# Kernel tuning notes

Hardware: AMD Instinct MI355X
Metric: run time of the kernel (lower is better)

Reference implementation:

```python
import jax, jax.numpy as jnp
import numpy as np

N, H, W = 8, 64, 64
CIN = 512    # latent_size_prev == conv_insize
COUT = 512   # latent_size == conv_outsize
Z = 512      # latent vector dim


def setup_inputs() -> dict:
    key = jax.random.key(0)
    ks = jax.random.split(key, 6)
    data = jax.random.normal(ks[0], (N, H, W, CIN), dtype=jnp.float32)
    latent = jax.random.normal(ks[1], (N, Z), dtype=jnp.float32)
    dense_w = jax.random.normal(ks[2], (Z, CIN), dtype=jnp.float32)
    dense_b = jnp.ones((CIN,), dtype=jnp.float32)  # ones_initializer per StyleBlock2
    conv_w = jax.random.normal(ks[3], (3, 3, CIN, COUT), dtype=jnp.float32)
    bias = jnp.zeros((1, 1, 1, COUT), dtype=jnp.float32)
    noise_coef = jnp.zeros((1, 1, 1, COUT), dtype=jnp.float32)
    noise = jax.random.normal(ks[4], (N, H, W, COUT), dtype=jnp.float32)
    return {"data": data, "latent": latent, "dense_w": dense_w, "dense_b": dense_b,
            "conv_w": conv_w, "bias": bias, "noise_coef": noise_coef, "noise": noise}


def reference(data, latent, dense_w, dense_b, conv_w, bias, noise_coef, noise):
    # ScaledDense: style vector s = latent @ (W * sqrt(2/Z)) + b
    dense_coef = jnp.sqrt(2.0 / Z).astype(data.dtype)
    s = latent @ (dense_w * dense_coef) + dense_b           # [N, CIN]

    # modulate input by style
    x = data * s[:, None, None, :]                          # [N,H,W,CIN]

    conv_coef = jnp.sqrt(2.0 / (CIN * 9)).astype(data.dtype)
    w = conv_w * conv_coef                                  # [3,3,CIN,COUT]
    y = jax.lax.conv_general_dilated(
        x, w, window_strides=(1, 1), padding='SAME',
        dimension_numbers=('NHWC', 'HWIO', 'NHWC'))         # [N,H,W,COUT]

    # demodulation: sum_{k,k,cin} (w * s)^2 == (s^2) @ sum_{k,k} w^2
    w2 = jnp.sum(w * w, axis=(0, 1))                        # [CIN, COUT]
    d = jax.lax.rsqrt((s * s) @ w2 + 1e-8)                  # [N, COUT]
    y = y * d[:, None, None, :]

    y = y + bias + noise * noise_coef
    return jnp.where(y >= 0, y, 0.2 * y)  # leaky relu, alpha=0.2
```

## Files before the change

kernel.cpp:

```cpp
#include <hip/hip_runtime.h>
#include <stdint.h>

typedef unsigned short ushort_t;
typedef unsigned int uint_t;
typedef __bf16 bf16x8 __attribute__((ext_vector_type(8)));
typedef float f32x4 __attribute__((ext_vector_type(4)));

#define C2F 0.02083333333333333f

__device__ __forceinline__ float bf2f(unsigned short u) {
  union { unsigned int i; float f; } v; v.i = ((unsigned int)u) << 16; return v.f;
}
__device__ __forceinline__ unsigned short f2bf(float f) {
  union { float f; unsigned int i; } v; v.f = f;
  unsigned int r = v.i + 0x7FFFu + ((v.i >> 16) & 1u);
  return (unsigned short)(r >> 16);
}
__device__ __forceinline__ bool bf_mode(const void* dense_b) {
  return *(const uint_t*)dense_b == 0x3F803F80u;
}
__device__ __forceinline__ void async16(const void* g, void* l) {
  __builtin_amdgcn_global_load_lds(
      (const __attribute__((address_space(1))) unsigned int*)g,
      (__attribute__((address_space(3))) unsigned int*)l, 16, 0, 0);
}

__global__ void k_style_p(const void* __restrict__ latent, const void* __restrict__ dw,
                          const void* __restrict__ db, float* __restrict__ sp) {
  const bool bf = bf_mode(db);
  int c = blockIdx.x * 256 + threadIdx.x;
  int n = blockIdx.y, zc = blockIdx.z;
  int z0 = zc * 64;
  float acc = 0.f;
  if (bf) {
    const ushort_t* L = (const ushort_t*)latent;
    const ushort_t* W = (const ushort_t*)dw;
    for (int z = z0; z < z0 + 64; ++z) acc += bf2f(L[n * 512 + z]) * bf2f(W[z * 512 + c]);
  } else {
    const float* L = (const float*)latent;
    const float* W = (const float*)dw;
    for (int z = z0; z < z0 + 64; ++z) acc += L[n * 512 + z] * W[z * 512 + c];
  }
  sp[(zc * 8 + n) * 512 + c] = acc;
}

__global__ void k_style_f(const float* __restrict__ sp, const void* __restrict__ db,
                          float* __restrict__ s) {
  const bool bf = bf_mode(db);
  int c = blockIdx.x * 256 + threadIdx.x;
  int n = blockIdx.y;
  float acc = 0.f;
#pragma unroll
  for (int zc = 0; zc < 8; ++zc) acc += sp[(zc * 8 + n) * 512 + c];
  float bv = bf ? bf2f(((const ushort_t*)db)[c]) : ((const float*)db)[c];
  s[n * 512 + c] = acc * 0.0625f + bv;
}

__global__ void k_w2(const void* __restrict__ cw, const void* __restrict__ db,
                     float* __restrict__ w2) {
  const bool bf = bf_mode(db);
  int i = blockIdx.x * blockDim.x + threadIdx.x;
  float a = 0.f;
  if (bf) {
    const ushort_t* W = (const ushort_t*)cw;
    for (int t = 0; t < 9; ++t) { float v = bf2f(W[t * 262144 + i]); a += v * v; }
  } else {
    const float* W = (const float*)cw;
    for (int t = 0; t < 9; ++t) { float v = W[t * 262144 + i]; a += v * v; }
  }
  w2[i] = a;
}

__global__ void k_demod_p(const float* __restrict__ s, const float* __restrict__ w2,
                          float* __restrict__ qp) {
  int c = blockIdx.x * 256 + threadIdx.x;
  int n = blockIdx.y, kc = blockIdx.z;
  int k0 = kc * 64;
  float q = 0.f;
  for (int k = k0; k < k0 + 64; ++k) {
    float sv = s[n * 512 + k];
    q += sv * sv * w2[k * 512 + c];
  }
  qp[(kc * 8 + n) * 512 + c] = q;
}

__global__ void k_demod_f(const float* __restrict__ qp, float* __restrict__ dfac) {
  int c = blockIdx.x * 256 + threadIdx.x;
  int n = blockIdx.y;
  float q = 0.f;
#pragma unroll
  for (int kc = 0; kc < 8; ++kc) q += qp[(kc * 8 + n) * 512 + c];
  dfac[n * 512 + c] = C2F * rsqrtf(C2F * C2F * q + 1e-8f);
}

__global__ void k_wt(const void* __restrict__ cw, const void* __restrict__ db,
                     ushort_t* __restrict__ wT) {
  __shared__ ushort_t tile[64][66];
  const bool bf = bf_mode(db);
  int tap = blockIdx.z;
  int ci0 = blockIdx.y * 64, co0 = blockIdx.x * 64;
  int col = threadIdx.x & 63, r0 = threadIdx.x >> 6;
  if (bf) {
    const ushort_t* src = (const ushort_t*)cw + tap * 262144;
    for (int r = r0; r < 64; r += 4) tile[r][col] = src[(ci0 + r) * 512 + co0 + col];
  } else {
    const float* src = (const float*)cw + tap * 262144;
    for (int r = r0; r < 64; r += 4) tile[r][col] = f2bf(src[(ci0 + r) * 512 + co0 + col]);
  }
  __syncthreads();
  ushort_t* dst = wT + tap * 262144;
  for (int r = r0; r < 64; r += 4)
    dst[(co0 + r) * 512 + ci0 + col] = tile[col][r];
}

__global__ void k_xpad(const void* __restrict__ data, const void* __restrict__ db,
                       const float* __restrict__ s, ushort_t* __restrict__ xpad) {
  const bool bf = bf_mode(db);
  int idx = blockIdx.x * blockDim.x + threadIdx.x;
  int cpair = idx & 255;
  int p = idx >> 8;
  int wp = p % 66; int q = p / 66; int hp = q % 66; int n = q / 66;
  uint_t outv = 0u;
  if ((unsigned)(hp - 1) < 64u && (unsigned)(wp - 1) < 64u) {
    int c = cpair * 2;
    int src = ((n * 64 + (hp - 1)) * 64 + (wp - 1)) * 512 + c;
    float s0 = s[n * 512 + c], s1 = s[n * 512 + c + 1];
    float x0, x1;
    if (bf) {
      uint_t dp = *(const uint_t*)((const ushort_t*)data + src);
      x0 = bf2f((unsigned short)(dp & 0xFFFFu)) * s0;
      x1 = bf2f((unsigned short)(dp >> 16)) * s1;
    } else {
      const float* df = (const float*)data;
      x0 = df[src] * s0;
      x1 = df[src + 1] * s1;
    }
    outv = (uint_t)f2bf(x0) | ((uint_t)f2bf(x1) << 16);
  }
  *(uint_t*)(xpad + idx * 2) = outv;
}

template <bool BF>
__device__ __forceinline__ void do_epilogue(
    const f32x4 (&acc)[4][4], const float* __restrict__ dfac,
    const void* __restrict__ bias, const void* __restrict__ ncoef,
    const void* __restrict__ noise, void* __restrict__ out,
    int n_img, int posBase, int coutBase, int lane, int wm, int wn) {
  const int rowq = (lane >> 4) * 4;
#pragma unroll
  for (int j = 0; j < 4; ++j) {
    const int cout = coutBase + wn + j * 16 + (lane & 15);
    const float dv = dfac[n_img * 512 + cout];
    const float bv = BF ? bf2f(((const ushort_t*)bias)[cout]) : ((const float*)bias)[cout];
    const float nc = BF ? bf2f(((const ushort_t*)ncoef)[cout]) : ((const float*)ncoef)[cout];
#pragma unroll
    for (int i = 0; i < 4; ++i) {
      const int m = wm + i * 16 + rowq;
#pragma unroll
      for (int r = 0; r < 4; ++r) {
        const size_t o = (size_t)(posBase + m + r) * 512 + cout;
        const float nv = BF ? bf2f(((const ushort_t*)noise)[o]) : ((const float*)noise)[o];
        float y = acc[i][j][r] * dv + bv + nv * nc;
        y = (y >= 0.f) ? y : 0.2f * y;
        if (BF) ((ushort_t*)out)[o] = f2bf(y);
        else    ((float*)out)[o] = y;
      }
    }
  }
}

__global__ __launch_bounds__(256, 2) void k_conv(
    const ushort_t* __restrict__ xpad, const ushort_t* __restrict__ wT,
    const float* __restrict__ dfac, const void* __restrict__ bias,
    const void* __restrict__ ncoef, const void* __restrict__ noise,
    const void* __restrict__ db, void* __restrict__ out) {
  __shared__ ushort_t Asm[128 * 32];
  __shared__ ushort_t Bsm[128 * 32];

  const int t = threadIdx.x;
  const int bid = blockIdx.x;
  const int xcd = bid & 7;
  const int slot = bid >> 3;
  const int coutBase = (slot & 3) * 128;
  const int posBase = ((slot >> 2) + 32 * xcd) * 128;
  const int n_img = posBase >> 12;

  const int prow = t >> 2;
  const int kch = (t & 3) * 8;
  const int pos0 = posBase + prow;
  const int pos1 = pos0 + 64;
  const int h0 = (pos0 >> 6) & 63, w0c = pos0 & 63;
  const int h1 = (pos1 >> 6) & 63, w1c = pos1 & 63;
  const ushort_t* gA0 = xpad + ((n_img * 66 + h0) * 66 + w0c) * 512 + kch;
  const ushort_t* gA1 = xpad + ((n_img * 66 + h1) * 66 + w1c) * 512 + kch;
  const ushort_t* gB0 = wT + (coutBase + prow) * 512 + kch;
  const ushort_t* gB1 = gB0 + 64 * 512;
  ushort_t* lA0 = Asm + t * 8;
  ushort_t* lA1 = lA0 + 64 * 32;
  ushort_t* lB0 = Bsm + t * 8;
  ushort_t* lB1 = lB0 + 64 * 32;

  const int lane = t & 63;
  const int wm = ((t >> 7) & 1) * 64;
  const int wn = ((t >> 6) & 1) * 64;
  const int mrow = lane & 15;
  const int kreg = (lane >> 4) * 8;

  f32x4 acc[4][4] = {};

  for (int tap = 0; tap < 9; ++tap) {
    const int kh = tap / 3, kw = tap - kh * 3;
    const ushort_t* pA0 = gA0 + (kh * 66 + kw) * 512;
    const ushort_t* pA1 = gA1 + (kh * 66 + kw) * 512;
    const ushort_t* pB0 = gB0 + tap * 262144;
    const ushort_t* pB1 = gB1 + tap * 262144;
    for (int k0 = 0; k0 < 512; k0 += 32) {
      async16(pA0 + k0, lA0);
      async16(pA1 + k0, lA1);
      async16(pB0 + k0, lB0);
      async16(pB1 + k0, lB1);
      asm volatile("s_waitcnt vmcnt(0)" ::: "memory");
      __syncthreads();
      bf16x8 av[4], bv[4];
#pragma unroll
      for (int i = 0; i < 4; ++i)
        av[i] = *(const bf16x8*)(Asm + (wm + i * 16 + mrow) * 32 + kreg);
#pragma unroll
      for (int j = 0; j < 4; ++j)
        bv[j] = *(const bf16x8*)(Bsm + (wn + j * 16 + mrow) * 32 + kreg);
#pragma unroll
      for (int i = 0; i < 4; ++i)
#pragma unroll
        for (int j = 0; j < 4; ++j)
          acc[i][j] = __builtin_amdgcn_mfma_f32_16x16x32_bf16(av[i], bv[j], acc[i][j], 0, 0, 0);
      __syncthreads();
    }
  }

  if (bf_mode(db))
    do_epilogue<true>(acc, dfac, bias, ncoef, noise, out, n_img, posBase, coutBase, lane, wm, wn);
  else
    do_epilogue<false>(acc, dfac, bias, ncoef, noise, out, n_img, posBase, coutBase, lane, wm, wn);
}

extern "C" void kernel_launch(void* const* d_in, const int* in_sizes, int n_in,
                              void* d_out, int out_size, void* d_ws, size_t ws_size,
                              hipStream_t stream) {
  (void)in_sizes; (void)n_in; (void)out_size; (void)ws_size;
  const void* data    = d_in[0];
  const void* latent  = d_in[1];
  const void* dense_w = d_in[2];
  const void* dense_b = d_in[3];
  const void* conv_w  = d_in[4];
  const void* bias    = d_in[5];
  const void* ncoef   = d_in[6];
  const void* noise   = d_in[7];

  float* s    = (float*)d_ws;
  float* dfac = s + 4096;
  float* w2   = dfac + 4096;
  float* sp   = w2 + 262144;
  float* qp   = sp + 32768;
  ushort_t* wT   = (ushort_t*)(qp + 32768);
  ushort_t* xpad = wT + 2359296;

  k_style_p<<<dim3(2, 8, 8), 256, 0, stream>>>(latent, dense_w, dense_b, sp);
  k_style_f<<<dim3(2, 8), 256, 0, stream>>>(sp, dense_b, s);
  k_w2<<<1024, 256, 0, stream>>>(conv_w, dense_b, w2);
  k_wt<<<dim3(8, 8, 9), 256, 0, stream>>>(conv_w, dense_b, wT);
  k_demod_p<<<dim3(2, 8, 8), 256, 0, stream>>>(s, w2, qp);
  k_demod_f<<<dim3(2, 8), 256, 0, stream>>>(qp, dfac);
  k_xpad<<<34848, 256, 0, stream>>>(data, dense_b, s, xpad);
  k_conv<<<1024, 256, 0, stream>>>(xpad, wT, dfac, bias, ncoef, noise, dense_b, d_out);
}
```

Baseline: 437.1 us.

## Rewrite implicit-GEMM conv with 256x256 tiles, double-buffered swizzled LDS pipeline

The conv kernel moves from 128x128 tiles with a single-buffered 32-wide K loop to 256x256 tiles across 8 waves. It uses K-steps of 64, double-buffered XOR-swizzled LDS (128KB dynamic), and interleaves async global-to-LDS staging with MFMA phases using partial vmcnt waits and setprio. The padded-input prep kernel is also vectorized to 8 channels per thread. The aim is to hide load latency, cut barrier stalls and raise data reuse. In exchange it uses much more LDS and registers, and launches only 256 blocks.

```diff
diff --git a/kernel.cpp b/kernel.cpp
--- a/kernel.cpp
+++ b/kernel.cpp
@@ -116,51 +116,63 @@
 __global__ void k_xpad(const void* __restrict__ data, const void* __restrict__ db,
                        const float* __restrict__ s, ushort_t* __restrict__ xpad) {
   const bool bf = bf_mode(db);
-  int idx = blockIdx.x * blockDim.x + threadIdx.x;
-  int cpair = idx & 255;
-  int p = idx >> 8;
+  int idx = blockIdx.x * 256 + threadIdx.x;
+  int c = (idx & 63) * 8;
+  int p = idx >> 6;
   int wp = p % 66; int q = p / 66; int hp = q % 66; int n = q / 66;
-  uint_t outv = 0u;
+  uint_t ov[4] = {0u, 0u, 0u, 0u};
   if ((unsigned)(hp - 1) < 64u && (unsigned)(wp - 1) < 64u) {
-    int c = cpair * 2;
-    int src = ((n * 64 + (hp - 1)) * 64 + (wp - 1)) * 512 + c;
-    float s0 = s[n * 512 + c], s1 = s[n * 512 + c + 1];
-    float x0, x1;
+    const float4 s0 = *(const float4*)(s + n * 512 + c);
+    const float4 s1 = *(const float4*)(s + n * 512 + c + 4);
+    size_t src = (size_t)((n * 64 + (hp - 1)) * 64 + (wp - 1)) * 512 + c;
+    float x[8];
     if (bf) {
-      uint_t dp = *(const uint_t*)((const ushort_t*)data + src);
-      x0 = bf2f((unsigned short)(dp & 0xFFFFu)) * s0;
-      x1 = bf2f((unsigned short)(dp >> 16)) * s1;
+      uint4 dv = *(const uint4*)((const ushort_t*)data + src);
+      x[0] = bf2f((unsigned short)(dv.x & 0xFFFFu)); x[1] = bf2f((unsigned short)(dv.x >> 16));
+      x[2] = bf2f((unsigned short)(dv.y & 0xFFFFu)); x[3] = bf2f((unsigned short)(dv.y >> 16));
+      x[4] = bf2f((unsigned short)(dv.z & 0xFFFFu)); x[5] = bf2f((unsigned short)(dv.z >> 16));
+      x[6] = bf2f((unsigned short)(dv.w & 0xFFFFu)); x[7] = bf2f((unsigned short)(dv.w >> 16));
     } else {
-      const float* df = (const float*)data;
-      x0 = df[src] * s0;
-      x1 = df[src + 1] * s1;
+      const float* df = (const float*)data + src;
+      float4 a = *(const float4*)df; float4 b = *(const float4*)(df + 4);
+      x[0] = a.x; x[1] = a.y; x[2] = a.z; x[3] = a.w;
+      x[4] = b.x; x[5] = b.y; x[6] = b.z; x[7] = b.w;
     }
-    outv = (uint_t)f2bf(x0) | ((uint_t)f2bf(x1) << 16);
-  }
-  *(uint_t*)(xpad + idx * 2) = outv;
+    float sv[8] = {s0.x, s0.y, s0.z, s0.w, s1.x, s1.y, s1.z, s1.w};
+#pragma unroll
+    for (int j = 0; j < 4; ++j)
+      ov[j] = (uint_t)f2bf(x[j * 2] * sv[j * 2]) |
+              ((uint_t)f2bf(x[j * 2 + 1] * sv[j * 2 + 1]) << 16);
+  }
+  uint4 o; o.x = ov[0]; o.y = ov[1]; o.z = ov[2]; o.w = ov[3];
+  *(uint4*)(xpad + (size_t)p * 512 + c) = o;
 }
 
 template <bool BF>
-__device__ __forceinline__ void do_epilogue(
-    const f32x4 (&acc)[4][4], const float* __restrict__ dfac,
+__device__ __forceinline__ void epi(
+    const f32x4 (&acc)[2][4][2][2], const float* __restrict__ dfac,
     const void* __restrict__ bias, const void* __restrict__ ncoef,
     const void* __restrict__ noise, void* __restrict__ out,
-    int n_img, int posBase, int coutBase, int lane, int wm, int wn) {
-  const int rowq = (lane >> 4) * 4;
-#pragma unroll
-  for (int j = 0; j < 4; ++j) {
-    const int cout = coutBase + wn + j * 16 + (lane & 15);
+    int n_img, int posBase, int coutBase, int lane, int wr, int wc) {
+  const int rq = (lane >> 4) * 4;
+#pragma unroll
+  for (int nh = 0; nh < 2; ++nh)
+#pragma unroll
+  for (int fn = 0; fn < 2; ++fn) {
+    const int cout = coutBase + wc * 64 + nh * 32 + fn * 16 + (lane & 15);
     const float dv = dfac[n_img * 512 + cout];
     const float bv = BF ? bf2f(((const ushort_t*)bias)[cout]) : ((const float*)bias)[cout];
     const float nc = BF ? bf2f(((const ushort_t*)ncoef)[cout]) : ((const float*)ncoef)[cout];
 #pragma unroll
-    for (int i = 0; i < 4; ++i) {
-      const int m = wm + i * 16 + rowq;
+    for (int mh = 0; mh < 2; ++mh)
+#pragma unroll
+    for (int f = 0; f < 4; ++f) {
+      const int m = wr * 128 + mh * 64 + f * 16 + rq;
 #pragma unroll
       for (int r = 0; r < 4; ++r) {
         const size_t o = (size_t)(posBase + m + r) * 512 + cout;
         const float nv = BF ? bf2f(((const ushort_t*)noise)[o]) : ((const float*)noise)[o];
-        float y = acc[i][j][r] * dv + bv + nv * nc;
+        float y = acc[mh][f][nh][fn][r] * dv + bv + nv * nc;
         y = (y >= 0.f) ? y : 0.2f * y;
         if (BF) ((ushort_t*)out)[o] = f2bf(y);
         else    ((float*)out)[o] = y;
@@ -169,78 +181,120 @@
   }
 }
 
-__global__ __launch_bounds__(256, 2) void k_conv(
+__global__ __launch_bounds__(512, 2) void k_conv(
     const ushort_t* __restrict__ xpad, const ushort_t* __restrict__ wT,
     const float* __restrict__ dfac, const void* __restrict__ bias,
     const void* __restrict__ ncoef, const void* __restrict__ noise,
     const void* __restrict__ db, void* __restrict__ out) {
-  __shared__ ushort_t Asm[128 * 32];
-  __shared__ ushort_t Bsm[128 * 32];
+  extern __shared__ ushort_t lds[];
 
   const int t = threadIdx.x;
   const int bid = blockIdx.x;
-  const int xcd = bid & 7;
-  const int slot = bid >> 3;
-  const int coutBase = (slot & 3) * 128;
-  const int posBase = ((slot >> 2) + 32 * xcd) * 128;
+  const int coutBase = (bid & 1) * 256;
+  const int posBase = (bid >> 1) * 256;
   const int n_img = posBase >> 12;
-
-  const int prow = t >> 2;
-  const int kch = (t & 3) * 8;
-  const int pos0 = posBase + prow;
-  const int pos1 = pos0 + 64;
-  const int h0 = (pos0 >> 6) & 63, w0c = pos0 & 63;
-  const int h1 = (pos1 >> 6) & 63, w1c = pos1 & 63;
-  const ushort_t* gA0 = xpad + ((n_img * 66 + h0) * 66 + w0c) * 512 + kch;
-  const ushort_t* gA1 = xpad + ((n_img * 66 + h1) * 66 + w1c) * 512 + kch;
-  const ushort_t* gB0 = wT + (coutBase + prow) * 512 + kch;
-  const ushort_t* gB1 = gB0 + 64 * 512;
-  ushort_t* lA0 = Asm + t * 8;
-  ushort_t* lA1 = lA0 + 64 * 32;
-  ushort_t* lB0 = Bsm + t * 8;
-  ushort_t* lB1 = lB0 + 64 * 32;
-
-  const int lane = t & 63;
-  const int wm = ((t >> 7) & 1) * 64;
-  const int wn = ((t >> 6) & 1) * 64;
-  const int mrow = lane & 15;
-  const int kreg = (lane >> 4) * 8;
-
-  f32x4 acc[4][4] = {};
-
-  for (int tap = 0; tap < 9; ++tap) {
-    const int kh = tap / 3, kw = tap - kh * 3;
-    const ushort_t* pA0 = gA0 + (kh * 66 + kw) * 512;
-    const ushort_t* pA1 = gA1 + (kh * 66 + kw) * 512;
-    const ushort_t* pB0 = gB0 + tap * 262144;
-    const ushort_t* pB1 = gB1 + tap * 262144;
-    for (int k0 = 0; k0 < 512; k0 += 32) {
-      async16(pA0 + k0, lA0);
-      async16(pA1 + k0, lA1);
-      async16(pB0 + k0, lB0);
-      async16(pB1 + k0, lB1);
-      asm volatile("s_waitcnt vmcnt(0)" ::: "memory");
-      __syncthreads();
-      bf16x8 av[4], bv[4];
-#pragma unroll
-      for (int i = 0; i < 4; ++i)
-        av[i] = *(const bf16x8*)(Asm + (wm + i * 16 + mrow) * 32 + kreg);
-#pragma unroll
-      for (int j = 0; j < 4; ++j)
-        bv[j] = *(const bf16x8*)(Bsm + (wn + j * 16 + mrow) * 32 + kreg);
-#pragma unroll
-      for (int i = 0; i < 4; ++i)
-#pragma unroll
-        for (int j = 0; j < 4; ++j)
-          acc[i][j] = __builtin_amdgcn_mfma_f32_16x16x32_bf16(av[i], bv[j], acc[i][j], 0, 0, 0);
-      __syncthreads();
-    }
-  }
+  const int hh0 = (posBase >> 6) & 63;
+
+  const int rt = t >> 3;
+  const int c8 = ((t & 7) ^ (rt & 7)) * 8;
+  const ushort_t* aPtr = xpad + ((size_t)((n_img * 66 + hh0) * 66 + rt) * 512 + c8);
+  const int bRow = ((t >> 8) & 1) * 64 + ((t >> 3) & 31);
+  const ushort_t* bPtr = wT + ((size_t)(coutBase + bRow) * 512 + c8);
+  ushort_t* aLds = lds + t * 8;
+  ushort_t* bLds = lds + 32768 + t * 8;
+
+#define STG_A(slot, mh, kt) do { \
+    const int tap_ = (kt) >> 3, kh_ = tap_ / 3, kw_ = tap_ - kh_ * 3, k0_ = ((kt) & 7) << 6; \
+    async16(aPtr + ((((mh) + kh_) * 66 + kw_) * 512 + k0_), \
+            aLds + (slot) * 16384 + (mh) * 4096); \
+    async16(aPtr + ((((mh) + 2 + kh_) * 66 + kw_) * 512 + k0_), \
+            aLds + (slot) * 16384 + ((mh) + 2) * 4096); \
+  } while (0)
+#define STG_B(slot, nh, kt) do { \
+    const int tap_ = (kt) >> 3, k0_ = ((kt) & 7) << 6; \
+    async16(bPtr + (tap_ * 262144 + (nh) * 16384 + k0_), \
+            bLds + (slot) * 16384 + (nh) * 8192); \
+    async16(bPtr + (tap_ * 262144 + (nh) * 16384 + 65536 + k0_), \
+            bLds + (slot) * 16384 + (nh) * 8192 + 4096); \
+  } while (0)
+
+  STG_A(0, 0, 0); STG_B(0, 0, 0); STG_B(0, 1, 0); STG_A(0, 1, 0);
+  STG_A(1, 0, 1); STG_B(1, 0, 1); STG_B(1, 1, 1);
+
+  const int lane = t & 63, wid = t >> 6, wr = wid >> 2, wc = wid & 3;
+  const int g16 = (lane >> 4) * 16, lrow = lane & 15, xv = (lane & 7) << 4;
+  const char* LB = (const char*)lds;
+  const int sbA0 = (((wr * 128 + lrow) * 128) + g16) ^ xv;
+  const int sbA1 = (((wr * 128 + lrow) * 128) + 64 + g16) ^ xv;
+  const int sbB0 = ((65536 + (wc * 32 + lrow) * 128) + g16) ^ xv;
+  const int sbB1 = ((65536 + (wc * 32 + lrow) * 128) + 64 + g16) ^ xv;
+
+  bf16x8 rA[4][2], rB0[2][2], rB1[2][2];
+  f32x4 acc[2][4][2][2] = {};
+
+#define LDA(mh, sB) do { _Pragma("unroll") for (int f = 0; f < 4; ++f) { \
+    rA[f][0] = *(const bf16x8*)(LB + ((sB) + (mh) * 8192 + f * 2048 + sbA0)); \
+    rA[f][1] = *(const bf16x8*)(LB + ((sB) + (mh) * 8192 + f * 2048 + sbA1)); } } while (0)
+#define LDB(R, nh, sB) do { _Pragma("unroll") for (int fn = 0; fn < 2; ++fn) { \
+    R[fn][0] = *(const bf16x8*)(LB + ((sB) + (nh) * 16384 + fn * 2048 + sbB0)); \
+    R[fn][1] = *(const bf16x8*)(LB + ((sB) + (nh) * 16384 + fn * 2048 + sbB1)); } } while (0)
+#define MM(mh, nh, RB) do { __builtin_amdgcn_s_setprio(1); \
+    _Pragma("unroll") for (int f = 0; f < 4; ++f) \
+    _Pragma("unroll") for (int fn = 0; fn < 2; ++fn) \
+    _Pragma("unroll") for (int ks = 0; ks < 2; ++ks) \
+      acc[mh][f][nh][fn] = __builtin_amdgcn_mfma_f32_16x16x32_bf16( \
+          rA[f][ks], (RB)[fn][ks], acc[mh][f][nh][fn], 0, 0, 0); \
+    __builtin_amdgcn_s_setprio(0); } while (0)
+#define BAR()   asm volatile("s_barrier" ::: "memory")
+#define LGKM0() asm volatile("s_waitcnt lgkmcnt(0)" ::: "memory")
+#define WAITV6() asm volatile("s_waitcnt vmcnt(6)" ::: "memory")
+
+  WAITV6();
+  BAR();
+
+#pragma unroll 1
+  for (int it = 0; it < 36; ++it) {
+    const int kt0 = 2 * it;
+    const int ktA = kt0 + 1;
+    const int ktB = (kt0 + 2 <= 71) ? kt0 + 2 : 71;
+    const int ktC = (kt0 + 3 <= 71) ? kt0 + 3 : 71;
+    LDA(0, 0); LDB(rB0, 0, 0);
+    STG_A(1, 1, ktA);
+    BAR(); LGKM0(); MM(0, 0, rB0); BAR();
+    LDB(rB1, 1, 0);
+    STG_A(0, 0, ktB);
+    BAR(); LGKM0(); MM(0, 1, rB1); BAR();
+    LDA(1, 0);
+    STG_B(0, 0, ktB);
+    BAR(); LGKM0(); MM(1, 1, rB1); BAR();
+    STG_B(0, 1, ktB);
+    BAR(); MM(1, 0, rB0); WAITV6(); BAR();
+    LDA(0, 32768); LDB(rB0, 0, 32768);
+    STG_A(0, 1, ktB);
+    BAR(); LGKM0(); MM(0, 0, rB0); BAR();
+    LDB(rB1, 1, 32768);
+    STG_A(1, 0, ktC);
+    BAR(); LGKM0(); MM(0, 1, rB1); BAR();
+    LDA(1, 32768);
+    STG_B(1, 0, ktC);
+    BAR(); LGKM0(); MM(1, 1, rB1); BAR();
+    STG_B(1, 1, ktC);
+    BAR(); MM(1, 0, rB0); WAITV6(); BAR();
+  }
+  asm volatile("s_waitcnt vmcnt(0)" ::: "memory");
 
   if (bf_mode(db))
-    do_epilogue<true>(acc, dfac, bias, ncoef, noise, out, n_img, posBase, coutBase, lane, wm, wn);
+    epi<true>(acc, dfac, bias, ncoef, noise, out, n_img, posBase, coutBase, lane, wr, wc);
   else
-    do_epilogue<false>(acc, dfac, bias, ncoef, noise, out, n_img, posBase, coutBase, lane, wm, wn);
+    epi<false>(acc, dfac, bias, ncoef, noise, out, n_img, posBase, coutBase, lane, wr, wc);
+#undef STG_A
+#undef STG_B
+#undef LDA
+#undef LDB
+#undef MM
+#undef BAR
+#undef LGKM0
+#undef WAITV6
 }
 
 extern "C" void kernel_launch(void* const* d_in, const int* in_sizes, int n_in,
@@ -256,6 +310,13 @@
   const void* ncoef   = d_in[6];
   const void* noise   = d_in[7];
 
+  static int once = [] {
+    (void)hipFuncSetAttribute((const void*)k_conv,
+                              hipFuncAttributeMaxDynamicSharedMemorySize, 131072);
+    return 0;
+  }();
+  (void)once;
+
   float* s    = (float*)d_ws;
   float* dfac = s + 4096;
   float* w2   = dfac + 4096;
@@ -270,6 +331,6 @@
   k_wt<<<dim3(8, 8, 9), 256, 0, stream>>>(conv_w, dense_b, wT);
   k_demod_p<<<dim3(2, 8, 8), 256, 0, stream>>>(s, w2, qp);
   k_demod_f<<<dim3(2, 8), 256, 0, stream>>>(qp, dfac);
-  k_xpad<<<34848, 256, 0, stream>>>(data, dense_b, s, xpad);
-  k_conv<<<1024, 256, 0, stream>>>(xpad, wT, dfac, bias, ncoef, noise, dense_b, d_out);
-}
+  k_xpad<<<8712, 256, 0, stream>>>(data, dense_b, s, xpad);
+  k_conv<<<256, 512, 131072, stream>>>(xpad, wT, dfac, bias, ncoef, noise, dense_b, d_out);
+}
```

Result: faster. 397.7 us (-9.0%).
